# Performance work log

Hardware: AMD Instinct MI355X
Metric: run time of the kernel (lower is better)

Reference implementation:

```python
import jax, jax.numpy as jnp
import numpy as np

B = 16
COUNTS = np.array([6, 14, 10, 8, 16, 12, 9, 11, 7, 13, 10, 10, 8, 12, 6, 8], dtype=np.int64)  # sum=160, max=16
INPUT_DIM = 1024
D_IN = 834   # num_features_mixed4f + 2
G = 256      # num_features_gcn
NG = 4       # num_graphs
T, H, W = 8, 14, 14


def setup_inputs() -> dict:
    key = jax.random.key(0)
    ks = jax.random.split(key, 7)
    total = int(COUNTS.sum())
    return {
        "actor_features": jax.random.normal(ks[0], (total, INPUT_DIM), dtype=jnp.float32),
        "feature_map": jax.random.normal(ks[1], (B, D_IN, T, H, W), dtype=jnp.float32),
        "W_a": jax.random.normal(ks[2], (NG, G, INPUT_DIM), dtype=jnp.float32) * 0.02,
        "b_a": jnp.zeros((NG, G), dtype=jnp.float32),
        "W_c": jax.random.normal(ks[3], (NG, G, D_IN), dtype=jnp.float32) * 0.02,
        "b_c": jnp.zeros((NG, G), dtype=jnp.float32),
        "W_h": jax.random.normal(ks[4], (NG, G, G), dtype=jnp.float32) * 0.02,
        "num_actors_list": COUNTS,
        "return_features": 0,
    }


def _ragged_indices(counts):
    # static (concrete) ragged bookkeeping
    counts = np.asarray(counts)
    Bn = counts.shape[0]
    Nmax = int(counts.max())
    offsets = np.concatenate([np.zeros(1, np.int64), np.cumsum(counts)[:-1]])
    n = np.arange(Nmax)
    pad_idx = offsets[:, None] + np.minimum(n[None, :], counts[:, None] - 1)  # [B, Nmax]
    valid = (n[None, :] < counts[:, None])                                     # [B, Nmax]
    unpad_b = np.repeat(np.arange(Bn), counts)
    unpad_n = np.concatenate([np.arange(c) for c in counts])
    return pad_idx, valid, unpad_b, unpad_n


def reference(actor_features, feature_map, W_a, b_a, W_c, b_c, W_h,
              num_actors_list, return_features):
    pad_idx, valid, unpad_b, unpad_n = _ragged_indices(num_actors_list)
    valid_f = jnp.asarray(valid, actor_features.dtype)
    Bn = feature_map.shape[0]

    # actor embedding for all graphs: [total, ng, G]
    emb = jnp.einsum('td,gfd->tgf', actor_features, W_a) + b_a[None]
    # pad to [B, Nmax, ng, G]; zero padded slots (matches pad_sequence)
    padded = emb[pad_idx] * valid_f[:, :, None, None]

    # 1x1x1 conv == channel matmul over flattened spatio-temporal grid S=T*H*W
    fm = feature_map.reshape(Bn, feature_map.shape[1], -1)            # [B, C, S]
    ctx = jnp.einsum('bcs,gfc->bgfs', fm, W_c) + b_c[None, :, :, None]  # [B, ng, G, S]

    # adjacency: actor x context similarities, softmax over context locations
    adj = jnp.einsum('bngf,bgfs->bgns', padded, ctx)                  # [B, ng, Nmax, S]
    adj = jax.nn.softmax(adj, axis=-1)
    adj = adj * valid_f[:, None, :, None]                             # masked_fill pad rows -> 0

    # aggregate context + residual
    upd = jnp.einsum('bgns,bgfs->bngf', adj, ctx) + padded            # [B, Nmax, ng, G]

    # unpad back to ragged flat [total, ng, G] (dropout is identity in eval)
    flat = upd[unpad_b, unpad_n]
    out = jax.nn.relu(jnp.einsum('tgf,ghf->tgh', flat, W_h))          # head_linear + relu

    # func == 'concat': cat over graphs along feature dim -> [total, ng*G]
    return out.reshape(out.shape[0], -1)
```

## Files before the change

kernel.cpp:

```cpp
#include <hip/hip_runtime.h>

#define TOTAL   160
#define NMAX    16
#define INDIM   1024
#define DIN     834
#define KPAD    864
#define GF      256
#define SS      1568
#define SPAD    1664
#define CROW    264

__constant__ int c_counts[16] = {6,14,10,8,16,12,9,11,7,13,10,10,8,12,6,8};
__constant__ int c_offs[16]   = {0,6,20,30,38,54,66,75,86,93,106,116,126,134,146,152};
__constant__ int c_t0[8] = {0, 6, 12, 18, 25, 31, 37, 43};
__constant__ int c_t1[8] = {6, 12, 18, 25, 31, 37, 43, 49};

using bf16x8 = __attribute__((ext_vector_type(8))) short;
using f32x4  = __attribute__((ext_vector_type(4))) float;
using f32x2  = __attribute__((ext_vector_type(2))) float;
using us4    = __attribute__((ext_vector_type(4))) unsigned short;

__device__ inline unsigned short f2bf(float f) {
  union { float f; unsigned u; } v; v.f = f;
  const unsigned u = v.u;
  return (unsigned short)((u + 0x7FFFu + ((u >> 16) & 1u)) >> 16);
}
__device__ inline float bf2f(unsigned short h) {
  union { unsigned u; float f; } v; v.u = ((unsigned)h) << 16; return v.f;
}

__device__ __forceinline__ void gload16(const unsigned short* g, unsigned short* l) {
  __builtin_amdgcn_global_load_lds(
      (const __attribute__((address_space(1))) unsigned int*)(g),
      (__attribute__((address_space(3))) unsigned int*)(l), 16, 0, 0);
}

__global__ __launch_bounds__(256) void prep_all(
    const float* __restrict__ actor, const float* __restrict__ Wa,
    const float* __restrict__ b_a, const float* __restrict__ Wc,
    const float* __restrict__ Wh, const float* __restrict__ fm,
    float* __restrict__ emb, unsigned short* __restrict__ emb_h,
    unsigned short* __restrict__ Ah, unsigned short* __restrict__ Wh_h,
    unsigned short* __restrict__ BhT)
{
  __shared__ float tile[64][33];
  __shared__ unsigned short As[64 * 40];
  __shared__ unsigned short Bs[64 * 40];
  const int bid = blockIdx.x, tid = threadIdx.x;

  if (bid < 48) {
    const int n0 = (bid & 15) * 64, m0 = (bid >> 4) * 64;
    const int wave = tid >> 6, lane = tid & 63;
    const int wm = (wave >> 1) * 32, wn = (wave & 1) * 32;
    const int quad = lane >> 4, lr = lane & 15;
    const int r = tid >> 2, ko = (tid & 3) * 8;
    const bool mval = (m0 + r < TOTAL);

    f32x4 acc[2][2];
    #pragma unroll
    for (int i = 0; i < 2; ++i)
      #pragma unroll
      for (int j = 0; j < 2; ++j) acc[i][j] = (f32x4){0.f, 0.f, 0.f, 0.f};

    const float4 zf4 = {0.f, 0.f, 0.f, 0.f};
    float4 ra0, ra1, rb0, rb1;
    ra0 = mval ? *reinterpret_cast<const float4*>(actor + (size_t)(m0 + r) * INDIM + ko) : zf4;
    ra1 = mval ? *reinterpret_cast<const float4*>(actor + (size_t)(m0 + r) * INDIM + ko + 4) : zf4;
    rb0 = *reinterpret_cast<const float4*>(Wa + (size_t)(n0 + r) * INDIM + ko);
    rb1 = *reinterpret_cast<const float4*>(Wa + (size_t)(n0 + r) * INDIM + ko + 4);

    for (int kt = 0; kt < 32; ++kt) {
      __syncthreads();
      {
        us4 a0, a1, b0, b1;
        a0[0]=f2bf(ra0.x); a0[1]=f2bf(ra0.y); a0[2]=f2bf(ra0.z); a0[3]=f2bf(ra0.w);
        a1[0]=f2bf(ra1.x); a1[1]=f2bf(ra1.y); a1[2]=f2bf(ra1.z); a1[3]=f2bf(ra1.w);
        b0[0]=f2bf(rb0.x); b0[1]=f2bf(rb0.y); b0[2]=f2bf(rb0.z); b0[3]=f2bf(rb0.w);
        b1[0]=f2bf(rb1.x); b1[1]=f2bf(rb1.y); b1[2]=f2bf(rb1.z); b1[3]=f2bf(rb1.w);
        *reinterpret_cast<us4*>(&As[r * 40 + ko])     = a0;
        *reinterpret_cast<us4*>(&As[r * 40 + ko + 4]) = a1;
        *reinterpret_cast<us4*>(&Bs[r * 40 + ko])     = b0;
        *reinterpret_cast<us4*>(&Bs[r * 40 + ko + 4]) = b1;
      }
      __syncthreads();
      if (kt < 31) {
        const int k0 = (kt + 1) * 32;
        ra0 = mval ? *reinterpret_cast<const float4*>(actor + (size_t)(m0 + r) * INDIM + k0 + ko) : zf4;
        ra1 = mval ? *reinterpret_cast<const float4*>(actor + (size_t)(m0 + r) * INDIM + k0 + ko + 4) : zf4;
        rb0 = *reinterpret_cast<const float4*>(Wa + (size_t)(n0 + r) * INDIM + k0 + ko);
        rb1 = *reinterpret_cast<const float4*>(Wa + (size_t)(n0 + r) * INDIM + k0 + ko + 4);
      }
      bf16x8 af[2], bfr[2];
      #pragma unroll
      for (int i = 0; i < 2; ++i)
        af[i] = *reinterpret_cast<const bf16x8*>(&As[(wm + i * 16 + lr) * 40 + quad * 8]);
      #pragma unroll
      for (int j = 0; j < 2; ++j)
        bfr[j] = *reinterpret_cast<const bf16x8*>(&Bs[(wn + j * 16 + lr) * 40 + quad * 8]);
      #pragma unroll
      for (int i = 0; i < 2; ++i)
        #pragma unroll
        for (int j = 0; j < 2; ++j)
          acc[i][j] = __builtin_amdgcn_mfma_f32_16x16x32_bf16(af[i], bfr[j], acc[i][j], 0, 0, 0);
    }

    #pragma unroll
    for (int i = 0; i < 2; ++i) {
      #pragma unroll
      for (int reg = 0; reg < 4; ++reg) {
        const int m = m0 + wm + i * 16 + quad * 4 + reg;
        if (m >= TOTAL) continue;
        #pragma unroll
        for (int j = 0; j < 2; ++j) {
          const int n = n0 + wn + j * 16 + lr;
          const float v = acc[i][j][reg] + b_a[n];
          emb[(size_t)m * INDIM + n] = v;
          emb_h[(size_t)m * INDIM + n] = f2bf(v);
        }
      }
    }
  } else if (bid < 3760) {
    const int pb = bid - 48;
    if (pb < 3456) {
      const int idx = pb * 256 + tid;
      const int k = idx % KPAD, gm = idx / KPAD;
      Ah[idx] = (k < DIN) ? f2bf(Wc[gm * DIN + k]) : (unsigned short)0;
    } else {
      const int i = (pb - 3456) * 256 + tid;
      const float4 v = reinterpret_cast<const float4*>(Wh)[i];
      us4 o; o[0] = f2bf(v.x); o[1] = f2bf(v.y); o[2] = f2bf(v.z); o[3] = f2bf(v.w);
      reinterpret_cast<us4*>(Wh_h)[i] = o;
    }
  } else {
    const int fb = bid - 3760;
    const int sx = fb % 49;
    const int ky = (fb / 49) % 14;
    const int b  = fb / (49 * 14);
    const int k0 = ky * 64, s0 = sx * 32;
    const int tx = tid & 31, ty = tid >> 5;
    const float* src = fm + (size_t)b * DIN * SS;
    #pragma unroll
    for (int r = 0; r < 8; ++r) {
      const int k = k0 + ty + r * 8;
      tile[ty + r * 8][tx] = (k < DIN) ? src[(size_t)k * SS + s0 + tx] : 0.f;
    }
    __syncthreads();
    const int srow = tid >> 3, kc = (tid & 7) * 8;
    if (k0 + kc < KPAD) {
      unsigned short* dst = BhT + (size_t)b * SS * KPAD + (size_t)(s0 + srow) * KPAD + k0 + kc;
      uint4 o;
      o.x = (unsigned)f2bf(tile[kc + 0][srow]) | ((unsigned)f2bf(tile[kc + 1][srow]) << 16);
      o.y = (unsigned)f2bf(tile[kc + 2][srow]) | ((unsigned)f2bf(tile[kc + 3][srow]) << 16);
      o.z = (unsigned)f2bf(tile[kc + 4][srow]) | ((unsigned)f2bf(tile[kc + 5][srow]) << 16);
      o.w = (unsigned)f2bf(tile[kc + 6][srow]) | ((unsigned)f2bf(tile[kc + 7][srow]) << 16);
      *reinterpret_cast<uint4*>(dst) = o;
    }
  }
}

__global__ __launch_bounds__(256, 3) void ctx_mfma(const unsigned short* __restrict__ Ah,
                                                   const unsigned short* __restrict__ BhT,
                                                   const float* __restrict__ b_c,
                                                   unsigned short* __restrict__ ctxT) {
  __shared__ unsigned short ABuf[3][2][4096];
  const int lin  = blockIdx.x;
  const int xcd  = lin & 7;
  const int slot = lin >> 3;
  const int bloc = (slot >= 104) ? 1 : 0;
  const int within = slot - bloc * 104;
  const int b  = xcd * 2 + bloc;
  const int mt = within % 13;
  const int gn = within / 13;
  const int g  = gn & 3;
  const int n0 = (gn >> 2) * 128;
  const int m0 = mt * 128;
  const int zout = (g << 4) + b;

  const int tid = threadIdx.x;
  const int w = tid >> 6, lane = tid & 63;
  const int wm = (w >> 1) * 64, wn = (w & 1) * 64;
  const int quad = lane >> 4, lr = lane & 15;

  const unsigned short* Ag = BhT + (size_t)b * SS * KPAD + (size_t)m0 * KPAD;
  const unsigned short* Bg = Ah + (size_t)g * 256 * KPAD + (size_t)n0 * KPAD;

  int rS[2], kS[2];
  #pragma unroll
  for (int p = 0; p < 2; ++p) {
    const int o    = p * 4096 + w * 1024 + lane * 16;
    const int line = o >> 7;
    const int gs   = (o >> 4) & 7;
    const int gg   = gs ^ (line & 7);
    rS[p] = line * 2 + (gg >> 2);
    kS[p] = (gg & 3) * 8;
  }

  int offA[4], offB[4];
  #pragma unroll
  for (int i = 0; i < 4; ++i) {
    const int r = wm + i * 16 + lr;
    const int line = r >> 1;
    const int gs = ((r & 1) * 4 + quad) ^ (line & 7);
    offA[i] = line * 64 + gs * 8;
  }
  #pragma unroll
  for (int j = 0; j < 4; ++j) {
    const int r = wn + j * 16 + lr;
    const int line = r >> 1;
    const int gs = ((r & 1) * 4 + quad) ^ (line & 7);
    offB[j] = line * 64 + gs * 8;
  }

  f32x4 acc[4][4];
  #pragma unroll
  for (int i = 0; i < 4; ++i)
    #pragma unroll
    for (int j = 0; j < 4; ++j) acc[i][j] = (f32x4){0.f, 0.f, 0.f, 0.f};

#define CTX_ISSUE(KT, BUF) {                                                          \
    _Pragma("unroll")                                                                 \
    for (int p = 0; p < 2; ++p) {                                                     \
      gload16(Ag + (size_t)rS[p] * KPAD + (KT) * 32 + kS[p],                          \
              &ABuf[BUF][0][p * 2048 + w * 512]);                                     \
      gload16(Bg + (size_t)rS[p] * KPAD + (KT) * 32 + kS[p],                          \
              &ABuf[BUF][1][p * 2048 + w * 512]);                                     \
    } }

#define CTX_BODY(KT, BUF, WAITSTR, DOISSUE) {                                         \
    asm volatile(WAITSTR ::: "memory");                                               \
    __builtin_amdgcn_s_barrier();                \
    bf16x8 af[4], bv[4];                                                              \
    _Pragma("unroll")                                                                 \
    for (int j = 0; j < 4; ++j)                                                       \
      bv[j] = *reinterpret_cast<const bf16x8*>(&ABuf[BUF][1][offB[j]]);               \
    _Pragma("unroll")                                                                 \
    for (int i = 0; i < 4; ++i)                                                       \
      af[i] = *reinterpret_cast<const bf16x8*>(&ABuf[BUF][0][offA[i]]);               \
    asm volatile("s_waitcnt lgkmcnt(0)" ::: "memory");                                \
    __builtin_amdgcn_sched_barrier(0);                                                \
    __builtin_amdgcn_s_barrier();                      \
    if (DOISSUE) CTX_ISSUE((KT) + 3, BUF);              \
    _Pragma("unroll")                                                                 \
    for (int i = 0; i < 4; ++i)                                                       \
      _Pragma("unroll")                                                               \
      for (int j = 0; j < 4; ++j)                                                     \
        acc[i][j] = __builtin_amdgcn_mfma_f32_16x16x32_bf16(af[i], bv[j], acc[i][j], 0, 0, 0); \
  }

  CTX_ISSUE(0, 0);
  CTX_ISSUE(1, 1);
  CTX_ISSUE(2, 2);

  for (int kt = 0; kt < 24; kt += 3) {
    CTX_BODY(kt,     0, "s_waitcnt vmcnt(8)", 1);
    CTX_BODY(kt + 1, 1, "s_waitcnt vmcnt(8)", 1);
    CTX_BODY(kt + 2, 2, "s_waitcnt vmcnt(8)", 1);
  }
  CTX_BODY(24, 0, "s_waitcnt vmcnt(8)", 0);
  CTX_BODY(25, 1, "s_waitcnt vmcnt(4)", 0);
  CTX_BODY(26, 2, "s_waitcnt vmcnt(0)", 0);

#undef CTX_BODY
#undef CTX_ISSUE

  unsigned short* Cz = ctxT + (size_t)zout * SPAD * GF;
  const float* bias = b_c + g * GF;
  float bvj[4];
  #pragma unroll
  for (int j = 0; j < 4; ++j) bvj[j] = bias[n0 + wn + j * 16 + lr];
  #pragma unroll
  for (int i = 0; i < 4; ++i) {
    #pragma unroll
    for (int reg = 0; reg < 4; ++reg) {
      const int m = m0 + wm + i * 16 + quad * 4 + reg;
      #pragma unroll
      for (int j = 0; j < 4; ++j) {
        Cz[(size_t)m * GF + n0 + wn + j * 16 + lr] = f2bf(acc[i][j][reg] + bvj[j]);
      }
    }
  }
}

__global__ __launch_bounds__(256) void att_part(
    const unsigned short* __restrict__ ctxT,
    const unsigned short* __restrict__ emb_h,
    float* __restrict__ Opart,
    float* __restrict__ Spart)
{
  __shared__ unsigned short Cs[4][32 * CROW];
  __shared__ float Ps[4][32][20];
  __shared__ float walpha[4][16];
  __shared__ float wms[4][16], wls[4][16];
  const int sc = blockIdx.x, z = blockIdx.y;
  const int g = z >> 4, b = z & 15;
  const int count = c_counts[b], off = c_offs[b];
  const int t0 = c_t0[sc], t1 = c_t1[sc];
  const int tid = threadIdx.x, wave = tid >> 6, lane = tid & 63;
  const int quad = lane >> 4, lr = lane & 15;
  const unsigned short* Az = ctxT + (size_t)z * SPAD * GF;
  const bool bvalid = (lr < count);
  const unsigned short* Brow = emb_h + (size_t)(off + (bvalid ? lr : 0)) * INDIM + (g << 8);
  unsigned short* myC = &Cs[wave][0];
  const int fbase = quad * 64 + lr * 4;
  const bf16x8 zero8 = (bf16x8)(short)0;

  f32x2 O2[16][2];
  #pragma unroll
  for (int n = 0; n < 16; ++n) {
    O2[n][0] = (f32x2){0.f, 0.f};
    O2[n][1] = (f32x2){0.f, 0.f};
  }
  float m_run = -3.0e38f, l_run = 0.f;

  for (int t = t0 + wave; t < t1; t += 4) {
    const int s0 = t * 32;
    #pragma unroll
    for (int q = 0; q < 16; ++q) {
      const int row = 2 * q + (lane >> 5);
      const int col = (lane & 31) * 8;
      const uint4 v = *reinterpret_cast<const uint4*>(Az + (size_t)(s0 + row) * GF + col);
      *reinterpret_cast<uint4*>(&myC[row * CROW + col]) = v;
    }
    f32x4 acc[2] = {(f32x4){0.f,0.f,0.f,0.f}, (f32x4){0.f,0.f,0.f,0.f}};
    #pragma unroll
    for (int kk = 0; kk < 8; ++kk) {
      const int f = kk * 32 + quad * 8;
      bf16x8 bv8 = *reinterpret_cast<const bf16x8*>(Brow + f);
      if (!bvalid) bv8 = zero8;
      #pragma unroll
      for (int i = 0; i < 2; ++i) {
        const bf16x8 av8 = *reinterpret_cast<const bf16x8*>(&myC[(i * 16 + lr) * CROW + f]);
        acc[i] = __builtin_amdgcn_mfma_f32_16x16x32_bf16(av8, bv8, acc[i], 0, 0, 0);
      }
    }
    float mx = acc[0][0];
    #pragma unroll
    for (int i = 0; i < 2; ++i)
      #pragma unroll
      for (int r = 0; r < 4; ++r) mx = fmaxf(mx, acc[i][r]);
    float lsum = 0.f;
    #pragma unroll
    for (int i = 0; i < 2; ++i)
      #pragma unroll
      for (int r = 0; r < 4; ++r) lsum += __expf(acc[i][r] - mx);
    #pragma unroll
    for (int d = 16; d < 64; d <<= 1) {
      const float om = __shfl_xor(mx, d, 64);
      const float ol = __shfl_xor(lsum, d, 64);
      const float M = fmaxf(mx, om);
      lsum = lsum * __expf(mx - M) + ol * __expf(om - M);
      mx = M;
    }
    const float m_new = fmaxf(m_run, mx);
    const float alpha = __expf(m_run - m_new);
    const float beta  = __expf(mx - m_new);
    l_run = alpha * l_run + beta * lsum;
    m_run = m_new;
    if (lane < 16) walpha[wave][lane] = alpha;
    #pragma unroll
    for (int i = 0; i < 2; ++i)
      #pragma unroll
      for (int r = 0; r < 4; ++r) {
        const int sl = i * 16 + quad * 4 + r;
        Ps[wave][sl][lr] = beta * __expf(acc[i][r] - mx);
      }
    float av[16];
    {
      const float4 a0 = *reinterpret_cast<const float4*>(&walpha[wave][0]);
      const float4 a1 = *reinterpret_cast<const float4*>(&walpha[wave][4]);
      const float4 a2 = *reinterpret_cast<const float4*>(&walpha[wave][8]);
      const float4 a3 = *reinterpret_cast<const float4*>(&walpha[wave][12]);
      av[0]=a0.x; av[1]=a0.y; av[2]=a0.z; av[3]=a0.w;
      av[4]=a1.x; av[5]=a1.y; av[6]=a1.z; av[7]=a1.w;
      av[8]=a2.x; av[9]=a2.y; av[10]=a2.z; av[11]=a2.w;
      av[12]=a3.x; av[13]=a3.y; av[14]=a3.z; av[15]=a3.w;
    }
    #pragma unroll
    for (int q = 0; q < 4; ++q) {
      if (q * 4 < count) {
        #pragma unroll
        for (int nn = 0; nn < 4; ++nn) {
          const int n = q * 4 + nn;
          O2[n][0] *= av[n];
          O2[n][1] *= av[n];
        }
      }
    }
    for (int s = 0; s < 32; ++s) {
      const us4 cv = *reinterpret_cast<const us4*>(&myC[s * CROW + fbase]);
      const f32x2 c01 = {bf2f(cv[0]), bf2f(cv[1])};
      const f32x2 c23 = {bf2f(cv[2]), bf2f(cv[3])};
      #pragma unroll
      for (int q = 0; q < 4; ++q) {
        if (q * 4 < count) {
          const float4 p = *reinterpret_cast<const float4*>(&Ps[wave][s][q * 4]);
          const float pq[4] = {p.x, p.y, p.z, p.w};
          #pragma unroll
          for (int nn = 0; nn < 4; ++nn) {
            const int n = q * 4 + nn;
            O2[n][0] += pq[nn] * c01;
            O2[n][1] += pq[nn] * c23;
          }
        }
      }
    }
  }

  if (lane < 16) { wms[wave][lane] = m_run; wls[wave][lane] = l_run; }
  __syncthreads();
  float* Ob = reinterpret_cast<float*>(&Cs[wave][0]);
  #pragma unroll
  for (int n = 0; n < 16; ++n) {
    const float Mb = fmaxf(fmaxf(wms[0][n], wms[1][n]), fmaxf(wms[2][n], wms[3][n]));
    const float e = __expf(wms[wave][n] - Mb);
    Ob[n * 256 + fbase + 0] = O2[n][0][0] * e;
    Ob[n * 256 + fbase + 1] = O2[n][0][1] * e;
    Ob[n * 256 + fbase + 2] = O2[n][1][0] * e;
    Ob[n * 256 + fbase + 3] = O2[n][1][1] * e;
  }
  __syncthreads();
  float* Op = Opart + ((size_t)z * 8 + sc) * 4096;
  #pragma unroll
  for (int nn = 0; nn < 4; ++nn) {
    const int n = wave * 4 + nn;
    float4 v = {0.f, 0.f, 0.f, 0.f};
    #pragma unroll
    for (int w = 0; w < 4; ++w) {
      const float4 x = *reinterpret_cast<const float4*>(
          reinterpret_cast<const float*>(&Cs[w][0]) + n * 256 + fbase);
      v.x += x.x; v.y += x.y; v.z += x.z; v.w += x.w;
    }
    *reinterpret_cast<float4*>(Op + n * 256 + fbase) = v;
  }
  if (wave == 0 && lane < 16) {
    const int n = lane;
    const float Mb = fmaxf(fmaxf(wms[0][n], wms[1][n]), fmaxf(wms[2][n], wms[3][n]));
    float Lb = 0.f;
    #pragma unroll
    for (int w = 0; w < 4; ++w) Lb += wls[w][n] * __expf(wms[w][n] - Mb);
    Spart[((size_t)z * 8 + sc) * 32 + n]      = Mb;
    Spart[((size_t)z * 8 + sc) * 32 + 16 + n] = Lb;
  }
}

__global__ __launch_bounds__(256) void att_combine(
    const float* __restrict__ Opart, const float* __restrict__ Spart,
    const float* __restrict__ emb, unsigned short* __restrict__ flat_h) {
  const int z = blockIdx.x, n = blockIdx.y;
  const int g = z >> 4, b = z & 15;
  const int count = c_counts[b], off = c_offs[b];
  if (n >= count) return;
  const int f = threadIdx.x;
  float M = -3.0e38f;
  #pragma unroll
  for (int sc = 0; sc < 8; ++sc)
    M = fmaxf(M, Spart[((size_t)z * 8 + sc) * 32 + n]);
  float L = 0.f, acc = 0.f;
  #pragma unroll
  for (int sc = 0; sc < 8; ++sc) {
    const float e = __expf(Spart[((size_t)z * 8 + sc) * 32 + n] - M);
    L += e * Spart[((size_t)z * 8 + sc) * 32 + 16 + n];
    acc += e * Opart[((size_t)z * 8 + sc) * 4096 + n * 256 + f];
  }
  const int t = off + n;
  const int col = (g << 8) + f;
  flat_h[t * INDIM + col] = f2bf(acc / L + emb[t * INDIM + col]);
}

__global__ __launch_bounds__(256) void head_mfma(const unsigned short* __restrict__ flat_h,
                                                 const unsigned short* __restrict__ Wh_h,
                                                 float* __restrict__ out) {
  __shared__ unsigned short As[64 * 40];
  __shared__ unsigned short Bs[64 * 40];
  const int g = blockIdx.z;
  const int n0 = blockIdx.x * 64, m0 = blockIdx.y * 64;
  const int tid = threadIdx.x;
  const int wave = tid >> 6, lane = tid & 63;
  const int wm = (wave >> 1) * 32, wn = (wave & 1) * 32;
  const int quad = lane >> 4, lr = lane & 15;
  const int r = tid >> 2, ko = (tid & 3) * 8;

  const unsigned short* Ag = flat_h + (size_t)m0 * INDIM + g * GF;
  const unsigned short* Bg = Wh_h + (size_t)g * GF * GF + (size_t)n0 * GF;

  f32x4 acc[2][2];
  #pragma unroll
  for (int i = 0; i < 2; ++i)
    #pragma unroll
    for (int j = 0; j < 2; ++j) acc[i][j] = (f32x4){0.f, 0.f, 0.f, 0.f};

  const uint4 zero4 = {0u, 0u, 0u, 0u};
  uint4 ra, rb;
  ra = (m0 + r < TOTAL) ? *reinterpret_cast<const uint4*>(Ag + (size_t)r * INDIM + ko) : zero4;
  rb = *reinterpret_cast<const uint4*>(Bg + (size_t)r * GF + ko);

  for (int kt = 0; kt < 8; ++kt) {
    __syncthreads();
    *reinterpret_cast<uint4*>(&As[r * 40 + ko]) = ra;
    *reinterpret_cast<uint4*>(&Bs[r * 40 + ko]) = rb;
    __syncthreads();
    if (kt < 7) {
      const int k0 = (kt + 1) * 32;
      ra = (m0 + r < TOTAL) ? *reinterpret_cast<const uint4*>(Ag + (size_t)r * INDIM + k0 + ko) : zero4;
      rb = *reinterpret_cast<const uint4*>(Bg + (size_t)r * GF + k0 + ko);
    }
    bf16x8 af[2], bfr[2];
    #pragma unroll
    for (int i = 0; i < 2; ++i)
      af[i] = *reinterpret_cast<const bf16x8*>(&As[(wm + i * 16 + lr) * 40 + quad * 8]);
    #pragma unroll
    for (int j = 0; j < 2; ++j)
      bfr[j] = *reinterpret_cast<const bf16x8*>(&Bs[(wn + j * 16 + lr) * 40 + quad * 8]);
    #pragma unroll
    for (int i = 0; i < 2; ++i)
      #pragma unroll
      for (int j = 0; j < 2; ++j)
        acc[i][j] = __builtin_amdgcn_mfma_f32_16x16x32_bf16(af[i], bfr[j], acc[i][j], 0, 0, 0);
  }

  #pragma unroll
  for (int i = 0; i < 2; ++i) {
    #pragma unroll
    for (int reg = 0; reg < 4; ++reg) {
      const int m = m0 + wm + i * 16 + quad * 4 + reg;
      if (m >= TOTAL) continue;
      #pragma unroll
      for (int j = 0; j < 2; ++j) {
        const int n = n0 + wn + j * 16 + lr;
        out[(size_t)m * INDIM + g * GF + n] = fmaxf(acc[i][j][reg], 0.f);
      }
    }
  }
}

extern "C" void kernel_launch(void* const* d_in, const int* in_sizes, int n_in,
                              void* d_out, int out_size, void* d_ws, size_t ws_size,
                              hipStream_t stream) {
  (void)in_sizes; (void)n_in; (void)out_size; (void)ws_size;
  const float* actor = (const float*)d_in[0];
  const float* fmap  = (const float*)d_in[1];
  const float* W_a   = (const float*)d_in[2];
  const float* b_a   = (const float*)d_in[3];
  const float* W_c   = (const float*)d_in[4];
  const float* b_c   = (const float*)d_in[5];
  const float* W_h   = (const float*)d_in[6];
  float* out = (float*)d_out;
  char* ws = (char*)d_ws;

  float* emb             = (float*)(ws);
  unsigned short* flat_h = (unsigned short*)(ws + 655360);
  unsigned short* emb_h  = (unsigned short*)(ws + 983040);
  float* Spart           = (float*)(ws + 1310720);
  unsigned short* ctxT   = (unsigned short*)(ws + 1376256);
  unsigned short* Ah     = (unsigned short*)(ws + 55902208);
  unsigned short* BhT    = (unsigned short*)(ws + 57671680);
  float* Opart           = (float*)(ws + 57671680);
  unsigned short* Wh_h   = (unsigned short*)(ws + 101023744);

  hipLaunchKernelGGL(prep_all, dim3(14736), dim3(256), 0, stream,
                     actor, W_a, b_a, W_c, W_h, fmap,
                     emb, emb_h, Ah, Wh_h, BhT);

  hipLaunchKernelGGL(ctx_mfma, dim3(1664), dim3(256), 0, stream, Ah, BhT, b_c, ctxT);

  hipLaunchKernelGGL(att_part, dim3(8, 64), dim3(256), 0, stream,
                     ctxT, emb_h, Opart, Spart);

  hipLaunchKernelGGL(att_combine, dim3(64, 16), dim3(256), 0, stream,
                     Opart, Spart, emb, flat_h);

  hipLaunchKernelGGL(head_mfma, dim3(4, 3, 4), dim3(256), 0, stream,
                     flat_h, Wh_h, out);
}
```

Before: 275.2 us.

## Fuse attention combine into head GEMM and widen feature-map transpose tiles

The feature-map transpose/convert blocks now load 32 channel rows by 224 spatial positions with float4 reads into a larger shared tile. Each block writes more bf16 output, and far fewer blocks are launched. Separately, the att_combine kernel is folded into the head GEMM. Each head block rebuilds its 64-row slice of combined attention plus residual in shared memory, which removes one launch and the flat_h round trip. The cost is redundant combine work across the four n-tiles of the head, and larger LDS usage that can lower occupancy.

```diff
diff --git a/kernel.cpp b/kernel.cpp
--- a/kernel.cpp
+++ b/kernel.cpp
@@ -15,6 +15,41 @@
 __constant__ int c_t0[8] = {0, 6, 12, 18, 25, 31, 37, 43};
 __constant__ int c_t1[8] = {6, 12, 18, 25, 31, 37, 43, 49};
 
+__constant__ unsigned char c_b_of_t[160] = {
+  0,0,0,0,0,0,
+  1,1,1,1,1,1,1,1,1,1,1,1,1,1,
+  2,2,2,2,2,2,2,2,2,2,
+  3,3,3,3,3,3,3,3,
+  4,4,4,4,4,4,4,4,4,4,4,4,4,4,4,4,
+  5,5,5,5,5,5,5,5,5,5,5,5,
+  6,6,6,6,6,6,6,6,6,
+  7,7,7,7,7,7,7,7,7,7,7,
+  8,8,8,8,8,8,8,
+  9,9,9,9,9,9,9,9,9,9,9,9,9,
+  10,10,10,10,10,10,10,10,10,10,
+  11,11,11,11,11,11,11,11,11,11,
+  12,12,12,12,12,12,12,12,
+  13,13,13,13,13,13,13,13,13,13,13,13,
+  14,14,14,14,14,14,
+  15,15,15,15,15,15,15,15};
+__constant__ unsigned char c_n_of_t[160] = {
+  0,1,2,3,4,5,
+  0,1,2,3,4,5,6,7,8,9,10,11,12,13,
+  0,1,2,3,4,5,6,7,8,9,
+  0,1,2,3,4,5,6,7,
+  0,1,2,3,4,5,6,7,8,9,10,11,12,13,14,15,
+  0,1,2,3,4,5,6,7,8,9,10,11,
+  0,1,2,3,4,5,6,7,8,
+  0,1,2,3,4,5,6,7,8,9,10,
+  0,1,2,3,4,5,6,
+  0,1,2,3,4,5,6,7,8,9,10,11,12,
+  0,1,2,3,4,5,6,7,8,9,
+  0,1,2,3,4,5,6,7,8,9,
+  0,1,2,3,4,5,6,7,
+  0,1,2,3,4,5,6,7,8,9,10,11,
+  0,1,2,3,4,5,
+  0,1,2,3,4,5,6,7};
+
 using bf16x8 = __attribute__((ext_vector_type(8))) short;
 using f32x4  = __attribute__((ext_vector_type(4))) float;
 using f32x2  = __attribute__((ext_vector_type(2))) float;
@@ -43,7 +78,7 @@
     unsigned short* __restrict__ Ah, unsigned short* __restrict__ Wh_h,
     unsigned short* __restrict__ BhT)
 {
-  __shared__ float tile[64][33];
+  __shared__ float tile[32][228];
   __shared__ unsigned short As[64 * 40];
   __shared__ unsigned short Bs[64 * 40];
   const int bid = blockIdx.x, tid = threadIdx.x;
@@ -133,27 +168,32 @@
     }
   } else {
     const int fb = bid - 3760;
-    const int sx = fb % 49;
-    const int ky = (fb / 49) % 14;
-    const int b  = fb / (49 * 14);
-    const int k0 = ky * 64, s0 = sx * 32;
-    const int tx = tid & 31, ty = tid >> 5;
-    const float* src = fm + (size_t)b * DIN * SS;
-    #pragma unroll
-    for (int r = 0; r < 8; ++r) {
-      const int k = k0 + ty + r * 8;
-      tile[ty + r * 8][tx] = (k < DIN) ? src[(size_t)k * SS + s0 + tx] : 0.f;
+    const int sx = fb % 7, ky = (fb / 7) % 27, b = fb / 189;
+    const int k0 = ky * 32, s0 = sx * 224;
+    const int r = tid >> 3, c8 = tid & 7;
+    const float* src = fm + (size_t)b * DIN * SS + (size_t)(k0 + r) * SS + s0;
+    const bool kv = (k0 + r < DIN);
+    const float4 zf = {0.f, 0.f, 0.f, 0.f};
+    #pragma unroll
+    for (int i = 0; i < 7; ++i) {
+      const int c4 = c8 + 8 * i;
+      const float4 v = kv ? *reinterpret_cast<const float4*>(src + c4 * 4) : zf;
+      *reinterpret_cast<float4*>(&tile[r][c4 * 4]) = v;
     }
     __syncthreads();
-    const int srow = tid >> 3, kc = (tid & 7) * 8;
-    if (k0 + kc < KPAD) {
-      unsigned short* dst = BhT + (size_t)b * SS * KPAD + (size_t)(s0 + srow) * KPAD + k0 + kc;
-      uint4 o;
-      o.x = (unsigned)f2bf(tile[kc + 0][srow]) | ((unsigned)f2bf(tile[kc + 1][srow]) << 16);
-      o.y = (unsigned)f2bf(tile[kc + 2][srow]) | ((unsigned)f2bf(tile[kc + 3][srow]) << 16);
-      o.z = (unsigned)f2bf(tile[kc + 4][srow]) | ((unsigned)f2bf(tile[kc + 5][srow]) << 16);
-      o.w = (unsigned)f2bf(tile[kc + 6][srow]) | ((unsigned)f2bf(tile[kc + 7][srow]) << 16);
-      *reinterpret_cast<uint4*>(dst) = o;
+    unsigned short* dstB = BhT + (size_t)b * SS * KPAD + (size_t)s0 * KPAD + k0;
+    #pragma unroll
+    for (int i = 0; i < 4; ++i) {
+      const int idx = tid + 256 * i;
+      if (idx < 896) {
+        const int s = idx >> 2, q = idx & 3;
+        uint4 o;
+        o.x = (unsigned)f2bf(tile[q*8+0][s]) | ((unsigned)f2bf(tile[q*8+1][s]) << 16);
+        o.y = (unsigned)f2bf(tile[q*8+2][s]) | ((unsigned)f2bf(tile[q*8+3][s]) << 16);
+        o.z = (unsigned)f2bf(tile[q*8+4][s]) | ((unsigned)f2bf(tile[q*8+5][s]) << 16);
+        o.w = (unsigned)f2bf(tile[q*8+6][s]) | ((unsigned)f2bf(tile[q*8+7][s]) << 16);
+        *reinterpret_cast<uint4*>(dstB + (size_t)s * KPAD + q * 8) = o;
+      }
     }
   }
 }
@@ -443,44 +483,55 @@
   }
 }
 
-__global__ __launch_bounds__(256) void att_combine(
+__global__ __launch_bounds__(256) void head_fused(
     const float* __restrict__ Opart, const float* __restrict__ Spart,
-    const float* __restrict__ emb, unsigned short* __restrict__ flat_h) {
-  const int z = blockIdx.x, n = blockIdx.y;
-  const int g = z >> 4, b = z & 15;
-  const int count = c_counts[b], off = c_offs[b];
-  if (n >= count) return;
-  const int f = threadIdx.x;
-  float M = -3.0e38f;
-  #pragma unroll
-  for (int sc = 0; sc < 8; ++sc)
-    M = fmaxf(M, Spart[((size_t)z * 8 + sc) * 32 + n]);
-  float L = 0.f, acc = 0.f;
-  #pragma unroll
-  for (int sc = 0; sc < 8; ++sc) {
-    const float e = __expf(Spart[((size_t)z * 8 + sc) * 32 + n] - M);
-    L += e * Spart[((size_t)z * 8 + sc) * 32 + 16 + n];
-    acc += e * Opart[((size_t)z * 8 + sc) * 4096 + n * 256 + f];
-  }
-  const int t = off + n;
-  const int col = (g << 8) + f;
-  flat_h[t * INDIM + col] = f2bf(acc / L + emb[t * INDIM + col]);
-}
-
-__global__ __launch_bounds__(256) void head_mfma(const unsigned short* __restrict__ flat_h,
-                                                 const unsigned short* __restrict__ Wh_h,
-                                                 float* __restrict__ out) {
-  __shared__ unsigned short As[64 * 40];
+    const float* __restrict__ emb, const unsigned short* __restrict__ Wh_h,
+    float* __restrict__ out)
+{
+  __shared__ unsigned short flatT[64 * 264];
   __shared__ unsigned short Bs[64 * 40];
   const int g = blockIdx.z;
   const int n0 = blockIdx.x * 64, m0 = blockIdx.y * 64;
   const int tid = threadIdx.x;
   const int wave = tid >> 6, lane = tid & 63;
+
+  for (int rr = 0; rr < 16; ++rr) {
+    const int m = wave + 4 * rr;
+    const int t = m0 + m;
+    const int f0 = lane * 4;
+    us4 o = {0, 0, 0, 0};
+    if (t < TOTAL) {
+      const int b = c_b_of_t[t], n = c_n_of_t[t];
+      const int z = (g << 4) + b;
+      float M = -3.0e38f;
+      #pragma unroll
+      for (int sc = 0; sc < 8; ++sc)
+        M = fmaxf(M, Spart[((size_t)z * 8 + sc) * 32 + n]);
+      float L = 0.f;
+      float4 a = {0.f, 0.f, 0.f, 0.f};
+      #pragma unroll
+      for (int sc = 0; sc < 8; ++sc) {
+        const float e = __expf(Spart[((size_t)z * 8 + sc) * 32 + n] - M);
+        L += e * Spart[((size_t)z * 8 + sc) * 32 + 16 + n];
+        const float4 op = *reinterpret_cast<const float4*>(
+            Opart + ((size_t)z * 8 + sc) * 4096 + n * 256 + f0);
+        a.x += e * op.x; a.y += e * op.y; a.z += e * op.z; a.w += e * op.w;
+      }
+      const float4 ev = *reinterpret_cast<const float4*>(
+          emb + (size_t)t * INDIM + (g << 8) + f0);
+      const float rL = 1.f / L;
+      o[0] = f2bf(a.x * rL + ev.x);
+      o[1] = f2bf(a.y * rL + ev.y);
+      o[2] = f2bf(a.z * rL + ev.z);
+      o[3] = f2bf(a.w * rL + ev.w);
+    }
+    *reinterpret_cast<us4*>(&flatT[m * 264 + f0]) = o;
+  }
+  __syncthreads();
+
   const int wm = (wave >> 1) * 32, wn = (wave & 1) * 32;
   const int quad = lane >> 4, lr = lane & 15;
   const int r = tid >> 2, ko = (tid & 3) * 8;
-
-  const unsigned short* Ag = flat_h + (size_t)m0 * INDIM + g * GF;
   const unsigned short* Bg = Wh_h + (size_t)g * GF * GF + (size_t)n0 * GF;
 
   f32x4 acc[2][2];
@@ -489,25 +540,20 @@
     #pragma unroll
     for (int j = 0; j < 2; ++j) acc[i][j] = (f32x4){0.f, 0.f, 0.f, 0.f};
 
-  const uint4 zero4 = {0u, 0u, 0u, 0u};
-  uint4 ra, rb;
-  ra = (m0 + r < TOTAL) ? *reinterpret_cast<const uint4*>(Ag + (size_t)r * INDIM + ko) : zero4;
-  rb = *reinterpret_cast<const uint4*>(Bg + (size_t)r * GF + ko);
+  uint4 rb = *reinterpret_cast<const uint4*>(Bg + (size_t)r * GF + ko);
 
   for (int kt = 0; kt < 8; ++kt) {
     __syncthreads();
-    *reinterpret_cast<uint4*>(&As[r * 40 + ko]) = ra;
     *reinterpret_cast<uint4*>(&Bs[r * 40 + ko]) = rb;
     __syncthreads();
     if (kt < 7) {
       const int k0 = (kt + 1) * 32;
-      ra = (m0 + r < TOTAL) ? *reinterpret_cast<const uint4*>(Ag + (size_t)r * INDIM + k0 + ko) : zero4;
       rb = *reinterpret_cast<const uint4*>(Bg + (size_t)r * GF + k0 + ko);
     }
     bf16x8 af[2], bfr[2];
     #pragma unroll
     for (int i = 0; i < 2; ++i)
-      af[i] = *reinterpret_cast<const bf16x8*>(&As[(wm + i * 16 + lr) * 40 + quad * 8]);
+      af[i] = *reinterpret_cast<const bf16x8*>(&flatT[(wm + i * 16 + lr) * 264 + kt * 32 + quad * 8]);
     #pragma unroll
     for (int j = 0; j < 2; ++j)
       bfr[j] = *reinterpret_cast<const bf16x8*>(&Bs[(wn + j * 16 + lr) * 40 + quad * 8]);
@@ -548,7 +594,6 @@
   char* ws = (char*)d_ws;
 
   float* emb             = (float*)(ws);
-  unsigned short* flat_h = (unsigned short*)(ws + 655360);
   unsigned short* emb_h  = (unsigned short*)(ws + 983040);
   float* Spart           = (float*)(ws + 1310720);
   unsigned short* ctxT   = (unsigned short*)(ws + 1376256);
@@ -557,7 +602,7 @@
   float* Opart           = (float*)(ws + 57671680);
   unsigned short* Wh_h   = (unsigned short*)(ws + 101023744);
 
-  hipLaunchKernelGGL(prep_all, dim3(14736), dim3(256), 0, stream,
+  hipLaunchKernelGGL(prep_all, dim3(6784), dim3(256), 0, stream,
                      actor, W_a, b_a, W_c, W_h, fmap,
                      emb, emb_h, Ah, Wh_h, BhT);
 
@@ -566,9 +611,6 @@
   hipLaunchKernelGGL(att_part, dim3(8, 64), dim3(256), 0, stream,
                      ctxT, emb_h, Opart, Spart);
 
-  hipLaunchKernelGGL(att_combine, dim3(64, 16), dim3(256), 0, stream,
-                     Opart, Spart, emb, flat_h);
-
-  hipLaunchKernelGGL(head_mfma, dim3(4, 3, 4), dim3(256), 0, stream,
-                     flat_h, Wh_h, out);
-}
+  hipLaunchKernelGGL(head_fused, dim3(4, 3, 4), dim3(256), 0, stream,
+                     Opart, Spart, emb, Wh_h, out);
+}
```

Result: slower. 290.0 us (+5.4%).
